# Kernel tuning notes

Measured on AMD Instinct MI355X. Metric: run time of the kernel, lower is better.

Reference implementation:

```python
import jax, jax.numpy as jnp
import numpy as np

N_NODES = 10000
N_EDGES = 320000
IN_FEATS = 128
HIDDEN = 128
NUM_CLASSES = 64


def setup_inputs() -> dict:
    key = jax.random.key(0)
    ks = jax.random.split(key, 16)
    edge_feats = jax.random.normal(ks[0], (N_EDGES, IN_FEATS), dtype=jnp.float32)
    src = jax.random.randint(ks[1], (N_EDGES,), 0, N_NODES, dtype=jnp.int32)
    dst = jax.random.randint(ks[2], (N_EDGES,), 0, N_NODES, dtype=jnp.int32)
    # guarantee every node has at least one in-edge (mean is well-defined)
    dst = dst.at[:N_NODES].set(jnp.arange(N_NODES, dtype=jnp.int32))
    def lin(k, fan_out, fan_in):
        s = 1.0 / np.sqrt(fan_in)
        kw, kb = jax.random.split(k)
        W = jax.random.uniform(kw, (fan_out, fan_in), jnp.float32, -s, s)
        b = jax.random.uniform(kb, (fan_out,), jnp.float32, -s, s)
        return W, b
    W1, b1 = lin(ks[3], HIDDEN, IN_FEATS)
    W2, b2 = lin(ks[4], HIDDEN, HIDDEN)
    W3, b3 = lin(ks[5], HIDDEN, HIDDEN)
    W4, b4 = lin(ks[6], HIDDEN, HIDDEN)
    W5, b5 = lin(ks[7], NUM_CLASSES, HIDDEN)
    return dict(edge_feats=edge_feats, src=src, dst=dst,
                W1=W1, b1=b1, W2=W2, b2=b2, W3=W3, b3=b3, W4=W4, b4=b4, W5=W5, b5=b5)


def _gcn_layer(edge_h, W, b, src, dst, in_deg):
    # (1) node h = mean of incoming edge features
    node_h = jax.ops.segment_sum(edge_h, dst, num_segments=N_NODES) / in_deg[:, None]
    # (2) send/recv: node h = sum over in-edges of src node h
    node_h = jax.ops.segment_sum(node_h[src], dst, num_segments=N_NODES)
    # (3) edge h = mean of endpoint node features
    edge_h = (node_h[src] + node_h[dst]) * 0.5
    # (4) dense linear on edge features
    return edge_h @ W.T + b


def reference(edge_feats, src, dst, W1, b1, W2, b2, W3, b3, W4, b4, W5, b5):
    in_deg = jax.ops.segment_sum(jnp.ones((N_EDGES,), jnp.float32), dst,
                                 num_segments=N_NODES)
    h = jax.nn.relu(_gcn_layer(edge_feats, W1, b1, src, dst, in_deg))
    h = jax.nn.relu(_gcn_layer(h, W2, b2, src, dst, in_deg))
    h = jax.nn.relu(_gcn_layer(h, W3, b3, src, dst, in_deg))
    h = jax.nn.relu(_gcn_layer(h, W4, b4, src, dst, in_deg))
    return _gcn_layer(h, W5, b5, src, dst, in_deg)
```

## Files before the change

### kernel.cpp

```cpp
#include <hip/hip_runtime.h>

#define NN 10000
#define NE 320000
#define F  128
#define BLK 256
#define CAP 96

__device__ __forceinline__ float bf2f(unsigned v16) {
    return __uint_as_float(v16 << 16);
}
__device__ __forceinline__ unsigned f2bf(float f) {
    unsigned u = __float_as_uint(f);
    return (u + 0x7FFFu + ((u >> 16) & 1u)) >> 16;
}
__device__ __forceinline__ unsigned pack2(float lo, float hi) {
    return f2bf(lo) | (f2bf(hi) << 16);
}
__device__ __forceinline__ void unpack8(uint4 q, float* v) {
    v[0] = bf2f(q.x & 0xffffu); v[1] = bf2f(q.x >> 16);
    v[2] = bf2f(q.y & 0xffffu); v[3] = bf2f(q.y >> 16);
    v[4] = bf2f(q.z & 0xffffu); v[5] = bf2f(q.z >> 16);
    v[6] = bf2f(q.w & 0xffffu); v[7] = bf2f(q.w >> 16);
}

__global__ void bucket_fill(const int* __restrict__ dst, const int* __restrict__ src,
                            int* __restrict__ cnt, int* __restrict__ buck,
                            int* __restrict__ bucksrc) {
    int e = blockIdx.x * 256 + threadIdx.x;
    if (e < NE) {
        int d = dst[e];
        int p = atomicAdd(&cnt[d], 1);
        buck[d * CAP + p]    = e;
        bucksrc[d * CAP + p] = src[e];
    }
}

__global__ __launch_bounds__(256) void seg_mean_k(const float4* __restrict__ ef,
                                                  const int* __restrict__ buck,
                                                  const int* __restrict__ cnt,
                                                  ushort4* __restrict__ Out) {
    __shared__ float4 red[8][32];
    int t  = threadIdx.x;
    int ns = t >> 7, es = (t >> 5) & 3, ch = t & 31;
    int n  = blockIdx.x * 2 + ns;
    int a = n * CAP, c = cnt[n], bnd = a + c;

    float ax = 0.f, ay = 0.f, az = 0.f, aw = 0.f;
    int i = a + es;
    for (; i + 12 < bnd; i += 16) {
        int s0 = buck[i], s1 = buck[i + 4], s2 = buck[i + 8], s3 = buck[i + 12];
        float4 v0 = ef[(size_t)s0 * 32 + ch];
        float4 v1 = ef[(size_t)s1 * 32 + ch];
        float4 v2 = ef[(size_t)s2 * 32 + ch];
        float4 v3 = ef[(size_t)s3 * 32 + ch];
        ax += v0.x + v1.x + v2.x + v3.x;
        ay += v0.y + v1.y + v2.y + v3.y;
        az += v0.z + v1.z + v2.z + v3.z;
        aw += v0.w + v1.w + v2.w + v3.w;
    }
    for (; i < bnd; i += 4) {
        float4 v0 = ef[(size_t)buck[i] * 32 + ch];
        ax += v0.x; ay += v0.y; az += v0.z; aw += v0.w;
    }

    red[t >> 5][ch] = make_float4(ax, ay, az, aw);
    __syncthreads();
    if (t < 64) {
        int ns2 = t >> 5, c2 = t & 31;
        float4 r0 = red[ns2 * 4 + 0][c2];
        float4 r1 = red[ns2 * 4 + 1][c2];
        float4 r2 = red[ns2 * 4 + 2][c2];
        float4 r3 = red[ns2 * 4 + 3][c2];
        int n2 = blockIdx.x * 2 + ns2;
        float sc = 1.0f / (float)cnt[n2];
        ushort4 o;
        o.x = (unsigned short)f2bf((r0.x + r1.x + r2.x + r3.x) * sc);
        o.y = (unsigned short)f2bf((r0.y + r1.y + r2.y + r3.y) * sc);
        o.z = (unsigned short)f2bf((r0.z + r1.z + r2.z + r3.z) * sc);
        o.w = (unsigned short)f2bf((r0.w + r1.w + r2.w + r3.w) * sc);
        Out[(size_t)n2 * 32 + c2] = o;
    }
}

__global__ __launch_bounds__(256) void relu_gather_k(const uint4* __restrict__ T,
                                                     const int* __restrict__ bucksrc,
                                                     const int* __restrict__ cnt,
                                                     const float* __restrict__ bias,
                                                     uint4* __restrict__ Out) {
    __shared__ float red[16][16][8];
    int t  = threadIdx.x;
    int ns = t >> 7, es = (t >> 4) & 7, ch = t & 15;
    int n  = blockIdx.x * 2 + ns;
    int a = n * CAP, bnd = a + cnt[n];

    float zn[8], bb[8], acc[8];
    unpack8(T[(size_t)n * 16 + ch], zn);
#pragma unroll
    for (int j = 0; j < 8; ++j) { bb[j] = bias[ch * 8 + j]; acc[j] = 0.f; }

    int i = a + es;
    for (; i + 24 < bnd; i += 32) {
        int s0 = bucksrc[i], s1 = bucksrc[i + 8], s2 = bucksrc[i + 16], s3 = bucksrc[i + 24];
        uint4 q0 = T[(size_t)s0 * 16 + ch];
        uint4 q1 = T[(size_t)s1 * 16 + ch];
        uint4 q2 = T[(size_t)s2 * 16 + ch];
        uint4 q3 = T[(size_t)s3 * 16 + ch];
        float v[8];
        unpack8(q0, v);
#pragma unroll
        for (int j = 0; j < 8; ++j) acc[j] += fmaxf(0.5f * (v[j] + zn[j]) + bb[j], 0.f);
        unpack8(q1, v);
#pragma unroll
        for (int j = 0; j < 8; ++j) acc[j] += fmaxf(0.5f * (v[j] + zn[j]) + bb[j], 0.f);
        unpack8(q2, v);
#pragma unroll
        for (int j = 0; j < 8; ++j) acc[j] += fmaxf(0.5f * (v[j] + zn[j]) + bb[j], 0.f);
        unpack8(q3, v);
#pragma unroll
        for (int j = 0; j < 8; ++j) acc[j] += fmaxf(0.5f * (v[j] + zn[j]) + bb[j], 0.f);
    }
    for (; i < bnd; i += 8) {
        uint4 q = T[(size_t)bucksrc[i] * 16 + ch];
        float v[8];
        unpack8(q, v);
#pragma unroll
        for (int j = 0; j < 8; ++j) acc[j] += fmaxf(0.5f * (v[j] + zn[j]) + bb[j], 0.f);
    }

#pragma unroll
    for (int j = 0; j < 8; ++j) red[t >> 4][ch][j] = acc[j];
    __syncthreads();
    if (t < 32) {
        int ns2 = t >> 4, c2 = t & 15;
        float s[8];
#pragma unroll
        for (int j = 0; j < 8; ++j) s[j] = 0.f;
#pragma unroll
        for (int sl = 0; sl < 8; ++sl)
#pragma unroll
            for (int j = 0; j < 8; ++j) s[j] += red[ns2 * 8 + sl][c2][j];
        int n2 = blockIdx.x * 2 + ns2;
        float sc = 1.0f / (float)cnt[n2];
        uint4 o;
        o.x = pack2(s[0] * sc, s[1] * sc);
        o.y = pack2(s[2] * sc, s[3] * sc);
        o.z = pack2(s[4] * sc, s[5] * sc);
        o.w = pack2(s[6] * sc, s[7] * sc);
        Out[(size_t)n2 * 16 + c2] = o;
    }
}

template <int OUT>
__global__ __launch_bounds__(256) void sum_gemm_k(const uint4* __restrict__ T,
                                                  const int* __restrict__ bucksrc,
                                                  const int* __restrict__ cnt,
                                                  const float* __restrict__ Wm,
                                                  unsigned short* __restrict__ Z) {
    __shared__ float red[16][16][8];
    __shared__ float xs[2][128];
    int t  = threadIdx.x;
    int ns = t >> 7, es = (t >> 4) & 7, ch = t & 15;
    int n  = blockIdx.x * 2 + ns;
    int a = n * CAP, bnd = a + cnt[n];

    float acc[8];
#pragma unroll
    for (int j = 0; j < 8; ++j) acc[j] = 0.f;

    int i = a + es;
    for (; i + 24 < bnd; i += 32) {
        int s0 = bucksrc[i], s1 = bucksrc[i + 8], s2 = bucksrc[i + 16], s3 = bucksrc[i + 24];
        uint4 q0 = T[(size_t)s0 * 16 + ch];
        uint4 q1 = T[(size_t)s1 * 16 + ch];
        uint4 q2 = T[(size_t)s2 * 16 + ch];
        uint4 q3 = T[(size_t)s3 * 16 + ch];
        float v[8];
        unpack8(q0, v);
#pragma unroll
        for (int j = 0; j < 8; ++j) acc[j] += v[j];
        unpack8(q1, v);
#pragma unroll
        for (int j = 0; j < 8; ++j) acc[j] += v[j];
        unpack8(q2, v);
#pragma unroll
        for (int j = 0; j < 8; ++j) acc[j] += v[j];
        unpack8(q3, v);
#pragma unroll
        for (int j = 0; j < 8; ++j) acc[j] += v[j];
    }
    for (; i < bnd; i += 8) {
        uint4 q = T[(size_t)bucksrc[i] * 16 + ch];
        float v[8];
        unpack8(q, v);
#pragma unroll
        for (int j = 0; j < 8; ++j) acc[j] += v[j];
    }

#pragma unroll
    for (int j = 0; j < 8; ++j) red[t >> 4][ch][j] = acc[j];
    __syncthreads();
    if (t < 32) {
        int ns2 = t >> 4, c2 = t & 15;
        float s[8];
#pragma unroll
        for (int j = 0; j < 8; ++j) s[j] = 0.f;
#pragma unroll
        for (int sl = 0; sl < 8; ++sl)
#pragma unroll
            for (int j = 0; j < 8; ++j) s[j] += red[ns2 * 8 + sl][c2][j];
#pragma unroll
        for (int j = 0; j < 8; ++j) xs[ns2][c2 * 8 + j] = s[j];
    }
    __syncthreads();

    if (t < OUT) {
        const float4* wrow = reinterpret_cast<const float4*>(&Wm[(size_t)t * 128]);
        float acc0 = 0.f, acc1 = 0.f;
#pragma unroll 8
        for (int k4 = 0; k4 < 32; ++k4) {
            float4 w  = wrow[k4];
            float4 x0 = *reinterpret_cast<const float4*>(&xs[0][k4 * 4]);
            float4 x1 = *reinterpret_cast<const float4*>(&xs[1][k4 * 4]);
            acc0 += w.x * x0.x + w.y * x0.y + w.z * x0.z + w.w * x0.w;
            acc1 += w.x * x1.x + w.y * x1.y + w.z * x1.z + w.w * x1.w;
        }
        Z[(size_t)(blockIdx.x * 2 + 0) * OUT + t] = (unsigned short)f2bf(acc0);
        Z[(size_t)(blockIdx.x * 2 + 1) * OUT + t] = (unsigned short)f2bf(acc1);
    }
}

__global__ __launch_bounds__(256) void edge_out(const uint4* __restrict__ z5,
                                                const float* __restrict__ b5,
                                                const int* __restrict__ src,
                                                const int* __restrict__ dst,
                                                float4* __restrict__ outp) {
    int t = blockIdx.x * 256 + threadIdx.x;
    int e = t >> 3, ch = t & 7;
    if (e < NE) {
        float va[8], vb[8];
        unpack8(z5[(size_t)src[e] * 8 + ch], va);
        unpack8(z5[(size_t)dst[e] * 8 + ch], vb);
        float4 r0, r1;
        r0.x = 0.5f * (va[0] + vb[0]) + b5[ch * 8 + 0];
        r0.y = 0.5f * (va[1] + vb[1]) + b5[ch * 8 + 1];
        r0.z = 0.5f * (va[2] + vb[2]) + b5[ch * 8 + 2];
        r0.w = 0.5f * (va[3] + vb[3]) + b5[ch * 8 + 3];
        r1.x = 0.5f * (va[4] + vb[4]) + b5[ch * 8 + 4];
        r1.y = 0.5f * (va[5] + vb[5]) + b5[ch * 8 + 5];
        r1.z = 0.5f * (va[6] + vb[6]) + b5[ch * 8 + 6];
        r1.w = 0.5f * (va[7] + vb[7]) + b5[ch * 8 + 7];
        outp[(size_t)e * 16 + ch * 2 + 0] = r0;
        outp[(size_t)e * 16 + ch * 2 + 1] = r1;
    }
}

extern "C" void kernel_launch(void* const* d_in, const int* in_sizes, int n_in,
                              void* d_out, int out_size, void* d_ws, size_t ws_size,
                              hipStream_t stream) {
    const float* ef  = (const float*)d_in[0];
    const int*   src = (const int*)d_in[1];
    const int*   dst = (const int*)d_in[2];
    const float* W1 = (const float*)d_in[3];  const float* b1 = (const float*)d_in[4];
    const float* W2 = (const float*)d_in[5];  const float* b2 = (const float*)d_in[6];
    const float* W3 = (const float*)d_in[7];  const float* b3 = (const float*)d_in[8];
    const float* W4 = (const float*)d_in[9];  const float* b4 = (const float*)d_in[10];
    const float* W5 = (const float*)d_in[11]; const float* b5 = (const float*)d_in[12];
    float* out = (float*)d_out;

    char* p = (char*)d_ws;
    auto alloc = [&](size_t bytes) {
        char* r = p;
        p += (bytes + 255) & ~(size_t)255;
        return r;
    };
    int* cnt     = (int*)alloc(NN * 4);
    int* buck    = (int*)alloc((size_t)NN * CAP * 4);
    int* bucksrc = (int*)alloc((size_t)NN * CAP * 4);
    unsigned short* m = (unsigned short*)alloc((size_t)NN * F * 2);
    unsigned short* z = (unsigned short*)alloc((size_t)NN * F * 2);

    hipMemsetAsync(cnt, 0, NN * 4, stream);
    bucket_fill<<<(NE + 255) / 256, 256, 0, stream>>>(dst, src, cnt, buck, bucksrc);

    const int GG = NN / 2;
    const uint4* m4 = (const uint4*)m;
    const uint4* z4 = (const uint4*)z;

    seg_mean_k<<<GG, BLK, 0, stream>>>((const float4*)ef, buck, cnt, (ushort4*)m);
    sum_gemm_k<128><<<GG, BLK, 0, stream>>>(m4, bucksrc, cnt, W1, z);

    const float* Wl[3] = {W2, W3, W4};
    const float* bl[3] = {b1, b2, b3};
    for (int L = 0; L < 3; ++L) {
        relu_gather_k<<<GG, BLK, 0, stream>>>(z4, bucksrc, cnt, bl[L], (uint4*)m);
        sum_gemm_k<128><<<GG, BLK, 0, stream>>>(m4, bucksrc, cnt, Wl[L], z);
    }

    relu_gather_k<<<GG, BLK, 0, stream>>>(z4, bucksrc, cnt, b4, (uint4*)m);
    sum_gemm_k<64><<<GG, BLK, 0, stream>>>(m4, bucksrc, cnt, W5, z);

    edge_out<<<(NE * 8 + 255) / 256, BLK, 0, stream>>>(z4, b5, src, dst, (float4*)out);
}
```

Baseline: 345.5 us.

## Map one wavefront per node in gather kernels with shuffle reductions

The relu_gather and sum_gemm kernels now assign one 64-lane wavefront per node, so each block handles four nodes instead of two. The cross-lane reduction uses __shfl_xor instead of shared memory plus __syncthreads, and the sum_gemm epilogue reuses each weight row across four node vectors. Gather loops are unrolled to eight outstanding loads per thread, in seg_mean_k as well. The aim is to cut shared-memory traffic and barriers and to raise memory-level parallelism and weight reuse, at the cost of fewer parallel edge slots per node.

New measurement: 286.2 us. -17.2%, faster.

```diff
diff --git a/kernel.cpp b/kernel.cpp
--- a/kernel.cpp
+++ b/kernel.cpp
@@ -43,27 +43,32 @@
     int t  = threadIdx.x;
     int ns = t >> 7, es = (t >> 5) & 3, ch = t & 31;
     int n  = blockIdx.x * 2 + ns;
-    int a = n * CAP, c = cnt[n], bnd = a + c;
+    int a = n * CAP, bnd = a + cnt[n];
 
     float ax = 0.f, ay = 0.f, az = 0.f, aw = 0.f;
     int i = a + es;
-    for (; i + 12 < bnd; i += 16) {
-        int s0 = buck[i], s1 = buck[i + 4], s2 = buck[i + 8], s3 = buck[i + 12];
+    for (; i + 28 < bnd; i += 32) {
+        int s0 = buck[i],      s1 = buck[i + 4],  s2 = buck[i + 8],  s3 = buck[i + 12];
+        int s4 = buck[i + 16], s5 = buck[i + 20], s6 = buck[i + 24], s7 = buck[i + 28];
         float4 v0 = ef[(size_t)s0 * 32 + ch];
         float4 v1 = ef[(size_t)s1 * 32 + ch];
         float4 v2 = ef[(size_t)s2 * 32 + ch];
         float4 v3 = ef[(size_t)s3 * 32 + ch];
-        ax += v0.x + v1.x + v2.x + v3.x;
-        ay += v0.y + v1.y + v2.y + v3.y;
-        az += v0.z + v1.z + v2.z + v3.z;
-        aw += v0.w + v1.w + v2.w + v3.w;
+        float4 v4 = ef[(size_t)s4 * 32 + ch];
+        float4 v5 = ef[(size_t)s5 * 32 + ch];
+        float4 v6 = ef[(size_t)s6 * 32 + ch];
+        float4 v7 = ef[(size_t)s7 * 32 + ch];
+        ax += v0.x + v1.x + v2.x + v3.x + v4.x + v5.x + v6.x + v7.x;
+        ay += v0.y + v1.y + v2.y + v3.y + v4.y + v5.y + v6.y + v7.y;
+        az += v0.z + v1.z + v2.z + v3.z + v4.z + v5.z + v6.z + v7.z;
+        aw += v0.w + v1.w + v2.w + v3.w + v4.w + v5.w + v6.w + v7.w;
     }
     for (; i < bnd; i += 4) {
         float4 v0 = ef[(size_t)buck[i] * 32 + ch];
         ax += v0.x; ay += v0.y; az += v0.z; aw += v0.w;
     }
 
-    red[t >> 5][ch] = make_float4(ax, ay, az, aw);
+    red[(t >> 5)][ch] = make_float4(ax, ay, az, aw);
     __syncthreads();
     if (t < 64) {
         int ns2 = t >> 5, c2 = t & 31;
@@ -87,10 +92,12 @@
                                                      const int* __restrict__ cnt,
                                                      const float* __restrict__ bias,
                                                      uint4* __restrict__ Out) {
-    __shared__ float red[16][16][8];
     int t  = threadIdx.x;
-    int ns = t >> 7, es = (t >> 4) & 7, ch = t & 15;
-    int n  = blockIdx.x * 2 + ns;
+    int nd = t >> 6;
+    int lane = t & 63;
+    int ch = lane & 15;
+    int es = lane >> 4;
+    int n  = blockIdx.x * 4 + nd;
     int a = n * CAP, bnd = a + cnt[n];
 
     float zn[8], bb[8], acc[8];
@@ -99,12 +106,17 @@
     for (int j = 0; j < 8; ++j) { bb[j] = bias[ch * 8 + j]; acc[j] = 0.f; }
 
     int i = a + es;
-    for (; i + 24 < bnd; i += 32) {
-        int s0 = bucksrc[i], s1 = bucksrc[i + 8], s2 = bucksrc[i + 16], s3 = bucksrc[i + 24];
+    for (; i + 28 < bnd; i += 32) {
+        int s0 = bucksrc[i],      s1 = bucksrc[i + 4],  s2 = bucksrc[i + 8],  s3 = bucksrc[i + 12];
+        int s4 = bucksrc[i + 16], s5 = bucksrc[i + 20], s6 = bucksrc[i + 24], s7 = bucksrc[i + 28];
         uint4 q0 = T[(size_t)s0 * 16 + ch];
         uint4 q1 = T[(size_t)s1 * 16 + ch];
         uint4 q2 = T[(size_t)s2 * 16 + ch];
         uint4 q3 = T[(size_t)s3 * 16 + ch];
+        uint4 q4 = T[(size_t)s4 * 16 + ch];
+        uint4 q5 = T[(size_t)s5 * 16 + ch];
+        uint4 q6 = T[(size_t)s6 * 16 + ch];
+        uint4 q7 = T[(size_t)s7 * 16 + ch];
         float v[8];
         unpack8(q0, v);
 #pragma unroll
@@ -118,8 +130,20 @@
         unpack8(q3, v);
 #pragma unroll
         for (int j = 0; j < 8; ++j) acc[j] += fmaxf(0.5f * (v[j] + zn[j]) + bb[j], 0.f);
-    }
-    for (; i < bnd; i += 8) {
+        unpack8(q4, v);
+#pragma unroll
+        for (int j = 0; j < 8; ++j) acc[j] += fmaxf(0.5f * (v[j] + zn[j]) + bb[j], 0.f);
+        unpack8(q5, v);
+#pragma unroll
+        for (int j = 0; j < 8; ++j) acc[j] += fmaxf(0.5f * (v[j] + zn[j]) + bb[j], 0.f);
+        unpack8(q6, v);
+#pragma unroll
+        for (int j = 0; j < 8; ++j) acc[j] += fmaxf(0.5f * (v[j] + zn[j]) + bb[j], 0.f);
+        unpack8(q7, v);
+#pragma unroll
+        for (int j = 0; j < 8; ++j) acc[j] += fmaxf(0.5f * (v[j] + zn[j]) + bb[j], 0.f);
+    }
+    for (; i < bnd; i += 4) {
         uint4 q = T[(size_t)bucksrc[i] * 16 + ch];
         float v[8];
         unpack8(q, v);
@@ -128,25 +152,19 @@
     }
 
 #pragma unroll
-    for (int j = 0; j < 8; ++j) red[t >> 4][ch][j] = acc[j];
-    __syncthreads();
-    if (t < 32) {
-        int ns2 = t >> 4, c2 = t & 15;
-        float s[8];
-#pragma unroll
-        for (int j = 0; j < 8; ++j) s[j] = 0.f;
-#pragma unroll
-        for (int sl = 0; sl < 8; ++sl)
-#pragma unroll
-            for (int j = 0; j < 8; ++j) s[j] += red[ns2 * 8 + sl][c2][j];
-        int n2 = blockIdx.x * 2 + ns2;
-        float sc = 1.0f / (float)cnt[n2];
+    for (int j = 0; j < 8; ++j) {
+        acc[j] += __shfl_xor(acc[j], 16, 64);
+        acc[j] += __shfl_xor(acc[j], 32, 64);
+    }
+
+    if (es == 0) {
+        float sc = 1.0f / (float)cnt[n];
         uint4 o;
-        o.x = pack2(s[0] * sc, s[1] * sc);
-        o.y = pack2(s[2] * sc, s[3] * sc);
-        o.z = pack2(s[4] * sc, s[5] * sc);
-        o.w = pack2(s[6] * sc, s[7] * sc);
-        Out[(size_t)n2 * 16 + c2] = o;
+        o.x = pack2(acc[0] * sc, acc[1] * sc);
+        o.y = pack2(acc[2] * sc, acc[3] * sc);
+        o.z = pack2(acc[4] * sc, acc[5] * sc);
+        o.w = pack2(acc[6] * sc, acc[7] * sc);
+        Out[(size_t)n * 16 + ch] = o;
     }
 }
 
@@ -156,11 +174,13 @@
                                                   const int* __restrict__ cnt,
                                                   const float* __restrict__ Wm,
                                                   unsigned short* __restrict__ Z) {
-    __shared__ float red[16][16][8];
-    __shared__ float xs[2][128];
+    __shared__ float xs[4][128];
     int t  = threadIdx.x;
-    int ns = t >> 7, es = (t >> 4) & 7, ch = t & 15;
-    int n  = blockIdx.x * 2 + ns;
+    int nd = t >> 6;
+    int lane = t & 63;
+    int ch = lane & 15;
+    int es = lane >> 4;
+    int n  = blockIdx.x * 4 + nd;
     int a = n * CAP, bnd = a + cnt[n];
 
     float acc[8];
@@ -168,12 +188,17 @@
     for (int j = 0; j < 8; ++j) acc[j] = 0.f;
 
     int i = a + es;
-    for (; i + 24 < bnd; i += 32) {
-        int s0 = bucksrc[i], s1 = bucksrc[i + 8], s2 = bucksrc[i + 16], s3 = bucksrc[i + 24];
+    for (; i + 28 < bnd; i += 32) {
+        int s0 = bucksrc[i],      s1 = bucksrc[i + 4],  s2 = bucksrc[i + 8],  s3 = bucksrc[i + 12];
+        int s4 = bucksrc[i + 16], s5 = bucksrc[i + 20], s6 = bucksrc[i + 24], s7 = bucksrc[i + 28];
         uint4 q0 = T[(size_t)s0 * 16 + ch];
         uint4 q1 = T[(size_t)s1 * 16 + ch];
         uint4 q2 = T[(size_t)s2 * 16 + ch];
         uint4 q3 = T[(size_t)s3 * 16 + ch];
+        uint4 q4 = T[(size_t)s4 * 16 + ch];
+        uint4 q5 = T[(size_t)s5 * 16 + ch];
+        uint4 q6 = T[(size_t)s6 * 16 + ch];
+        uint4 q7 = T[(size_t)s7 * 16 + ch];
         float v[8];
         unpack8(q0, v);
 #pragma unroll
@@ -187,8 +212,20 @@
         unpack8(q3, v);
 #pragma unroll
         for (int j = 0; j < 8; ++j) acc[j] += v[j];
-    }
-    for (; i < bnd; i += 8) {
+        unpack8(q4, v);
+#pragma unroll
+        for (int j = 0; j < 8; ++j) acc[j] += v[j];
+        unpack8(q5, v);
+#pragma unroll
+        for (int j = 0; j < 8; ++j) acc[j] += v[j];
+        unpack8(q6, v);
+#pragma unroll
+        for (int j = 0; j < 8; ++j) acc[j] += v[j];
+        unpack8(q7, v);
+#pragma unroll
+        for (int j = 0; j < 8; ++j) acc[j] += v[j];
+    }
+    for (; i < bnd; i += 4) {
         uint4 q = T[(size_t)bucksrc[i] * 16 + ch];
         float v[8];
         unpack8(q, v);
@@ -197,35 +234,36 @@
     }
 
 #pragma unroll
-    for (int j = 0; j < 8; ++j) red[t >> 4][ch][j] = acc[j];
-    __syncthreads();
-    if (t < 32) {
-        int ns2 = t >> 4, c2 = t & 15;
-        float s[8];
-#pragma unroll
-        for (int j = 0; j < 8; ++j) s[j] = 0.f;
-#pragma unroll
-        for (int sl = 0; sl < 8; ++sl)
-#pragma unroll
-            for (int j = 0; j < 8; ++j) s[j] += red[ns2 * 8 + sl][c2][j];
-#pragma unroll
-        for (int j = 0; j < 8; ++j) xs[ns2][c2 * 8 + j] = s[j];
+    for (int j = 0; j < 8; ++j) {
+        acc[j] += __shfl_xor(acc[j], 16, 64);
+        acc[j] += __shfl_xor(acc[j], 32, 64);
+    }
+    if (es == 0) {
+#pragma unroll
+        for (int j = 0; j < 8; ++j) xs[nd][ch * 8 + j] = acc[j];
     }
     __syncthreads();
 
     if (t < OUT) {
         const float4* wrow = reinterpret_cast<const float4*>(&Wm[(size_t)t * 128]);
-        float acc0 = 0.f, acc1 = 0.f;
+        float a0 = 0.f, a1 = 0.f, a2 = 0.f, a3 = 0.f;
 #pragma unroll 8
         for (int k4 = 0; k4 < 32; ++k4) {
             float4 w  = wrow[k4];
             float4 x0 = *reinterpret_cast<const float4*>(&xs[0][k4 * 4]);
             float4 x1 = *reinterpret_cast<const float4*>(&xs[1][k4 * 4]);
-            acc0 += w.x * x0.x + w.y * x0.y + w.z * x0.z + w.w * x0.w;
-            acc1 += w.x * x1.x + w.y * x1.y + w.z * x1.z + w.w * x1.w;
+            float4 x2 = *reinterpret_cast<const float4*>(&xs[2][k4 * 4]);
+            float4 x3 = *reinterpret_cast<const float4*>(&xs[3][k4 * 4]);
+            a0 += w.x * x0.x + w.y * x0.y + w.z * x0.z + w.w * x0.w;
+            a1 += w.x * x1.x + w.y * x1.y + w.z * x1.z + w.w * x1.w;
+            a2 += w.x * x2.x + w.y * x2.y + w.z * x2.z + w.w * x2.w;
+            a3 += w.x * x3.x + w.y * x3.y + w.z * x3.z + w.w * x3.w;
         }
-        Z[(size_t)(blockIdx.x * 2 + 0) * OUT + t] = (unsigned short)f2bf(acc0);
-        Z[(size_t)(blockIdx.x * 2 + 1) * OUT + t] = (unsigned short)f2bf(acc1);
+        int nb = blockIdx.x * 4;
+        Z[(size_t)(nb + 0) * OUT + t] = (unsigned short)f2bf(a0);
+        Z[(size_t)(nb + 1) * OUT + t] = (unsigned short)f2bf(a1);
+        Z[(size_t)(nb + 2) * OUT + t] = (unsigned short)f2bf(a2);
+        Z[(size_t)(nb + 3) * OUT + t] = (unsigned short)f2bf(a3);
     }
 }
 
@@ -282,22 +320,23 @@
     hipMemsetAsync(cnt, 0, NN * 4, stream);
     bucket_fill<<<(NE + 255) / 256, 256, 0, stream>>>(dst, src, cnt, buck, bucksrc);
 
-    const int GG = NN / 2;
+    const int G2 = NN / 2;
+    const int G4 = NN / 4;
     const uint4* m4 = (const uint4*)m;
     const uint4* z4 = (const uint4*)z;
 
-    seg_mean_k<<<GG, BLK, 0, stream>>>((const float4*)ef, buck, cnt, (ushort4*)m);
-    sum_gemm_k<128><<<GG, BLK, 0, stream>>>(m4, bucksrc, cnt, W1, z);
+    seg_mean_k<<<G2, BLK, 0, stream>>>((const float4*)ef, buck, cnt, (ushort4*)m);
+    sum_gemm_k<128><<<G4, BLK, 0, stream>>>(m4, bucksrc, cnt, W1, z);
 
     const float* Wl[3] = {W2, W3, W4};
     const float* bl[3] = {b1, b2, b3};
     for (int L = 0; L < 3; ++L) {
-        relu_gather_k<<<GG, BLK, 0, stream>>>(z4, bucksrc, cnt, bl[L], (uint4*)m);
-        sum_gemm_k<128><<<GG, BLK, 0, stream>>>(m4, bucksrc, cnt, Wl[L], z);
-    }
-
-    relu_gather_k<<<GG, BLK, 0, stream>>>(z4, bucksrc, cnt, b4, (uint4*)m);
-    sum_gemm_k<64><<<GG, BLK, 0, stream>>>(m4, bucksrc, cnt, W5, z);
+        relu_gather_k<<<G4, BLK, 0, stream>>>(z4, bucksrc, cnt, bl[L], (uint4*)m);
+        sum_gemm_k<128><<<G4, BLK, 0, stream>>>(m4, bucksrc, cnt, Wl[L], z);
+    }
+
+    relu_gather_k<<<G4, BLK, 0, stream>>>(z4, bucksrc, cnt, b4, (uint4*)m);
+    sum_gemm_k<64><<<G4, BLK, 0, stream>>>(m4, bucksrc, cnt, W5, z);
 
     edge_out<<<(NE * 8 + 255) / 256, BLK, 0, stream>>>(z4, b5, src, dst, (float4*)out);
 }
```
